# Kernel optimization log

Hardware: AMD Instinct MI355X
Metric: run time of the kernel (lower is better)

## Reference

```python
import jax, jax.numpy as jnp
import numpy as np

N_NODES = 100000
N_EDGES = 1600000
EMBED_DIM = 64


def setup_inputs() -> dict:
    key = jax.random.key(0)
    k1, k2, k3, k4 = jax.random.split(key, 4)
    ego_embeddings = jax.random.normal(k1, (N_NODES, EMBED_DIM), dtype=jnp.float32)
    adj_values = jax.random.uniform(k2, (N_EDGES,), dtype=jnp.float32)
    adj_rows = jax.random.randint(k3, (N_EDGES,), 0, N_NODES, dtype=jnp.int32)
    adj_cols = jax.random.randint(k4, (N_EDGES,), 0, N_NODES, dtype=jnp.int32)
    return {
        "ego_embeddings": ego_embeddings,
        "adj_values": adj_values,
        "adj_rows": adj_rows,
        "adj_cols": adj_cols,
    }


def reference(ego_embeddings, adj_values, adj_rows, adj_cols):
    # out[r, :] = sum_{e : rows[e]==r} values[e] * ego_embeddings[cols[e], :]
    # == tf.sparse.sparse_dense_matmul(adj, ego_embeddings)
    messages = adj_values[:, None] * ego_embeddings[adj_cols]  # [E, D]
    out = jax.ops.segment_sum(messages, adj_rows, num_segments=N_NODES)  # [N, D]
    return out
```

## Files before the change

### kernel.cpp

```cpp
#include <hip/hip_runtime.h>

#define N_NODES 100000
#define N_EDGES 1600000
#define EMBED_DIM 64

#define RPB 256
#define NBKT ((N_NODES + RPB - 1) / RPB)
#define CAP 4608
#define TILE 4096
#define NTILE ((N_EDGES + TILE - 1) / TILE)
#define OVCAP 8192

#define BG_THREADS 1024
#define EPT ((CAP + BG_THREADS - 1) / BG_THREADS)

__global__ __launch_bounds__(512) void k_binA(const int* __restrict__ rows,
                                              const int* __restrict__ cols,
                                              const float* __restrict__ vals,
                                              int* __restrict__ gcur,
                                              int2* __restrict__ packed,
                                              int* __restrict__ ov_cnt,
                                              int4* __restrict__ ov) {
    __shared__ int hist[NBKT];
    __shared__ int off[NBKT];
    __shared__ int cur[NBKT];
    __shared__ int gbase[NBKT];
    __shared__ int wsum[8];
    __shared__ int stotal;
    __shared__ int2 stage[TILE];
    __shared__ int dg[TILE];
    const int tid = threadIdx.x;
    const int lane = tid & 63;
    const int wid = tid >> 6;
    const int e0 = blockIdx.x * TILE;

    for (int i = tid; i < NBKT; i += 512) hist[i] = 0;
    __syncthreads();

    for (int i = tid; i < TILE; i += 512) {
        int e = e0 + i;
        if (e < N_EDGES) atomicAdd(&hist[rows[e] >> 8], 1);
    }
    __syncthreads();

    int v = (tid < NBKT) ? hist[tid] : 0;
    int incl = v;
    for (int o = 1; o < 64; o <<= 1) {
        int t = __shfl_up(incl, o, 64);
        if (lane >= o) incl += t;
    }
    if (lane == 63) wsum[wid] = incl;
    __syncthreads();
    if (wid == 0 && lane < 8) {
        int s = wsum[lane];
        int si = s;
        for (int o = 1; o < 8; o <<= 1) {
            int t = __shfl_up(si, o, 64);
            if (lane >= o) si += t;
        }
        wsum[lane] = si - s;
        if (lane == 7) stotal = si;
    }
    __syncthreads();
    int excl = incl - v + wsum[wid];
    if (tid < NBKT) { off[tid] = excl; cur[tid] = excl; }

    for (int b = tid; b < NBKT; b += 512) {
        int c = hist[b];
        gbase[b] = c ? atomicAdd(&gcur[b], c) : 0;
    }
    __syncthreads();

    for (int i = tid; i < TILE; i += 512) {
        int e = e0 + i;
        if (e < N_EDGES) {
            int r = rows[e];
            int b = r >> 8;
            int p = atomicAdd(&cur[b], 1);
            stage[p] = make_int2(((r & (RPB - 1)) << 17) | cols[e],
                                 __float_as_int(vals[e]));
            int d = gbase[b] + (p - off[b]);
            dg[p] = (d < CAP) ? (b * CAP + d) : (0x40000000 | b);
        }
    }
    __syncthreads();

    int total = stotal;
    for (int j = tid; j < total; j += 512) {
        int d = dg[j];
        int2 ev = stage[j];
        if (d & 0x40000000) {
            int b = d & 0xFFFF;
            int ovi = atomicAdd(ov_cnt, 1);
            if (ovi < OVCAP) {
                int r = b * RPB + (((unsigned)ev.x) >> 17);
                ov[ovi] = make_int4(r, ev.x & 0x1FFFF, ev.y, 0);
            }
        } else {
            packed[d] = ev;
        }
    }
}

__global__ __launch_bounds__(BG_THREADS) void k_bg(const float* __restrict__ x,
                                                   const int* __restrict__ gcur,
                                                   const int2* __restrict__ packed,
                                                   float* __restrict__ out) {
    __shared__ int2 stage[CAP];
    __shared__ int h[RPB];
    __shared__ int ofs[RPB];
    __shared__ int cur[RPB];
    __shared__ int wsum[4];
    const int b = blockIdx.x;
    const int tid = threadIdx.x;
    const int lane = tid & 63;
    const int wid = tid >> 6;
    int n = gcur[b];
    if (n > CAP) n = CAP;
    const int base = b * CAP;

    if (tid < RPB) h[tid] = 0;
    __syncthreads();

    int2 ereg[EPT];
    int lr[EPT];
#pragma unroll
    for (int jj = 0; jj < EPT; ++jj) {
        int j = tid + jj * BG_THREADS;
        lr[jj] = -1;
        if (j < n) {
            int2 e = packed[base + j];
            ereg[jj] = e;
            int r = ((unsigned)e.x) >> 17;
            lr[jj] = r;
            atomicAdd(&h[r], 1);
        }
    }
    __syncthreads();

    int hv = (tid < RPB) ? h[tid] : 0;
    int incl = hv;
    for (int o = 1; o < 64; o <<= 1) {
        int t = __shfl_up(incl, o, 64);
        if (lane >= o) incl += t;
    }
    if (tid < RPB && lane == 63) wsum[wid] = incl;
    __syncthreads();
    if (wid == 0 && lane < 4) {
        int s = wsum[lane];
        int si = s;
        for (int o = 1; o < 4; o <<= 1) {
            int t = __shfl_up(si, o, 64);
            if (lane >= o) si += t;
        }
        wsum[lane] = si - s;
    }
    __syncthreads();
    if (tid < RPB) {
        int o2 = incl - hv + wsum[wid];
        ofs[tid] = o2;
        cur[tid] = o2;
    }
    __syncthreads();

#pragma unroll
    for (int jj = 0; jj < EPT; ++jj) {
        if (lr[jj] >= 0) {
            int p = atomicAdd(&cur[lr[jj]], 1);
            stage[p] = ereg[jj];
        }
    }
    __syncthreads();

    const int half = lane >> 5;
    const int hl = lane & 31;
    const float2* __restrict__ x2 = (const float2*)x;
    for (int i = 0; i < 16; ++i) {
        int r = wid * 16 + i;
        int grow = b * RPB + r;
        if (grow >= N_NODES) break;
        int deg = h[r];
        int beg = ofs[r];
        float ax = 0.f, ay = 0.f;
        for (int j0 = 0; j0 < deg; j0 += 16) {
            float vv[8];
            float2 xv[8];
#pragma unroll
            for (int k = 0; k < 8; ++k) {
                int j = j0 + 2 * k + half;
                int2 e = (j < deg) ? stage[beg + j] : make_int2(0, 0);
                vv[k] = __int_as_float(e.y);
                xv[k] = x2[(e.x & 0x1FFFF) * 32 + hl];
            }
#pragma unroll
            for (int k = 0; k < 8; ++k) {
                ax += vv[k] * xv[k].x;
                ay += vv[k] * xv[k].y;
            }
        }
        ax += __shfl_xor(ax, 32);
        ay += __shfl_xor(ay, 32);
        if (half == 0) {
            ((float2*)out)[(size_t)grow * 32 + hl] = make_float2(ax, ay);
        }
    }
}

__global__ __launch_bounds__(256) void k_overflow(const float* __restrict__ x,
                                                  const int* __restrict__ ov_cnt,
                                                  const int4* __restrict__ ov,
                                                  float* __restrict__ out) {
    int n = *ov_cnt;
    if (n > OVCAP) n = OVCAP;
    int lane = threadIdx.x & 63;
    int wglobal = (blockIdx.x * 256 + threadIdx.x) >> 6;
    for (int i = wglobal; i < n; i += 64 * 4) {
        int4 e = ov[i];
        atomicAdd(&out[e.x * EMBED_DIM + lane],
                  __int_as_float(e.z) * x[e.y * EMBED_DIM + lane]);
    }
}

__global__ __launch_bounds__(256) void spmm_scatter_kernel(
    const float* __restrict__ x, const float* __restrict__ vals,
    const int* __restrict__ rows, const int* __restrict__ cols,
    float* __restrict__ out) {
    const int wave_in_block = threadIdx.x >> 6;
    const int lane = threadIdx.x & 63;
    const int e = blockIdx.x * 4 + wave_in_block;
    if (e >= N_EDGES) return;
    const float m = vals[e] * x[cols[e] * EMBED_DIM + lane];
    atomicAdd(&out[rows[e] * EMBED_DIM + lane], m);
}

extern "C" void kernel_launch(void* const* d_in, const int* in_sizes, int n_in,
                              void* d_out, int out_size, void* d_ws, size_t ws_size,
                              hipStream_t stream) {
    const float* x    = (const float*)d_in[0];
    const float* vals = (const float*)d_in[1];
    const int*   rows = (const int*)d_in[2];
    const int*   cols = (const int*)d_in[3];
    float* out = (float*)d_out;

    const size_t packed_b = (size_t)NBKT * CAP * 8;
    const size_t ov_b     = (size_t)OVCAP * 16;
    const size_t need = packed_b + ov_b + ((size_t)NBKT + 1) * 4;
    if (ws_size < need) {
        hipMemsetAsync(out, 0, (size_t)out_size * sizeof(float), stream);
        spmm_scatter_kernel<<<(N_EDGES + 3) / 4, 256, 0, stream>>>(x, vals, rows, cols, out);
        return;
    }

    int2* packed  = (int2*)d_ws;
    int4* ov      = (int4*)((char*)d_ws + packed_b);
    int*  gcur    = (int*)((char*)d_ws + packed_b + ov_b);
    int*  ov_cnt  = gcur + NBKT;

    hipMemsetAsync(gcur, 0, ((size_t)NBKT + 1) * sizeof(int), stream);

    k_binA<<<NTILE, 512, 0, stream>>>(rows, cols, vals, gcur, packed, ov_cnt, ov);
    k_bg<<<NBKT, BG_THREADS, 0, stream>>>(x, gcur, (const int2*)packed, out);
    k_overflow<<<64, 256, 0, stream>>>(x, ov_cnt, ov, out);
}
```

Before: 170.5 us.

## Fuse binning, bucket gather and overflow passes into one cooperative kernel

Replaces the memset plus three separate kernel launches with one cooperative kernel. It zeroes the counters, bins edges into row buckets and then runs the per-bucket gather, using grid-wide syncs between the phases. Each block now handles overflow edges for its own bucket, and the binning loads of rows, cols and vals are vectorized as int4/float4. This removes launch gaps and separate kernel boundaries. In exchange, all 391 blocks of 1024 threads must be co-resident, grid.sync has its own cost, and every block scans the whole overflow list. The old multi-kernel path is kept as a fallback if the cooperative launch fails.

```diff
diff --git a/kernel.cpp b/kernel.cpp
--- a/kernel.cpp
+++ b/kernel.cpp
@@ -1,4 +1,7 @@
 #include <hip/hip_runtime.h>
+#include <hip/hip_cooperative_groups.h>
+
+namespace cg = cooperative_groups;
 
 #define N_NODES 100000
 #define N_EDGES 1600000
@@ -10,9 +13,249 @@
 #define TILE 4096
 #define NTILE ((N_EDGES + TILE - 1) / TILE)
 #define OVCAP 8192
-
-#define BG_THREADS 1024
-#define EPT ((CAP + BG_THREADS - 1) / BG_THREADS)
+#define EPT 5
+
+#define SM_A_STAGE 6336
+#define SM_A_DG    (SM_A_STAGE + TILE * 8)
+#define SM_BYTES   (SM_A_DG + TILE * 4)
+#define SM_B_STAGE 3200
+
+__global__ __launch_bounds__(1024, 8) void k_fused(const int* __restrict__ rows,
+                                                   const int* __restrict__ cols,
+                                                   const float* __restrict__ vals,
+                                                   int* __restrict__ gcur,
+                                                   int2* __restrict__ packed,
+                                                   int* __restrict__ ov_cnt,
+                                                   int4* __restrict__ ov,
+                                                   const float* __restrict__ x,
+                                                   float* __restrict__ out) {
+    __shared__ __align__(16) char smem[SM_BYTES];
+    cg::grid_group grid = cg::this_grid();
+    const int tid = threadIdx.x;
+    const int lane = tid & 63;
+    const int wid = tid >> 6;
+    const int blk = blockIdx.x;
+
+    {
+        int gtid = blk * 1024 + tid;
+        if (gtid < NBKT + 1) gcur[gtid] = 0;
+    }
+    grid.sync();
+
+    {
+        int* hist  = (int*)smem;
+        int* off   = hist + NBKT;
+        int* cur   = off + NBKT;
+        int* gbase = cur + NBKT;
+        int* wsum  = gbase + NBKT;
+        int* stot  = wsum + 16;
+        int2* stage = (int2*)(smem + SM_A_STAGE);
+        int*  dg    = (int*)(smem + SM_A_DG);
+
+        for (int i = tid; i < NBKT; i += 1024) hist[i] = 0;
+        __syncthreads();
+
+        const int e0 = blk * TILE;
+        const int eb = e0 + 4 * tid;
+        int rr0 = -1, rr1 = -1, rr2 = -1, rr3 = -1;
+        if (eb + 3 < N_EDGES) {
+            int4 r4 = *(const int4*)(rows + eb);
+            rr0 = r4.x; rr1 = r4.y; rr2 = r4.z; rr3 = r4.w;
+        } else {
+            if (eb + 0 < N_EDGES) rr0 = rows[eb + 0];
+            if (eb + 1 < N_EDGES) rr1 = rows[eb + 1];
+            if (eb + 2 < N_EDGES) rr2 = rows[eb + 2];
+            if (eb + 3 < N_EDGES) rr3 = rows[eb + 3];
+        }
+        if (rr0 >= 0) atomicAdd(&hist[rr0 >> 8], 1);
+        if (rr1 >= 0) atomicAdd(&hist[rr1 >> 8], 1);
+        if (rr2 >= 0) atomicAdd(&hist[rr2 >> 8], 1);
+        if (rr3 >= 0) atomicAdd(&hist[rr3 >> 8], 1);
+        __syncthreads();
+
+        int v = (tid < NBKT) ? hist[tid] : 0;
+        int incl = v;
+        for (int o = 1; o < 64; o <<= 1) {
+            int t = __shfl_up(incl, o, 64);
+            if (lane >= o) incl += t;
+        }
+        if (lane == 63) wsum[wid] = incl;
+        __syncthreads();
+        if (wid == 0 && lane < 16) {
+            int s = wsum[lane];
+            int si = s;
+            for (int o = 1; o < 16; o <<= 1) {
+                int t = __shfl_up(si, o, 64);
+                if (lane >= o) si += t;
+            }
+            wsum[lane] = si - s;
+            if (lane == 15) *stot = si;
+        }
+        __syncthreads();
+        int excl = incl - v + wsum[wid];
+        if (tid < NBKT) { off[tid] = excl; cur[tid] = excl; }
+
+        for (int b = tid; b < NBKT; b += 1024) {
+            int c = hist[b];
+            gbase[b] = c ? atomicAdd(&gcur[b], c) : 0;
+        }
+        __syncthreads();
+
+        int cc0 = 0, cc1 = 0, cc2 = 0, cc3 = 0;
+        float vv0 = 0.f, vv1 = 0.f, vv2 = 0.f, vv3 = 0.f;
+        if (eb + 3 < N_EDGES) {
+            int4 c4 = *(const int4*)(cols + eb);
+            float4 v4 = *(const float4*)(vals + eb);
+            cc0 = c4.x; cc1 = c4.y; cc2 = c4.z; cc3 = c4.w;
+            vv0 = v4.x; vv1 = v4.y; vv2 = v4.z; vv3 = v4.w;
+        } else {
+            if (eb + 0 < N_EDGES) { cc0 = cols[eb + 0]; vv0 = vals[eb + 0]; }
+            if (eb + 1 < N_EDGES) { cc1 = cols[eb + 1]; vv1 = vals[eb + 1]; }
+            if (eb + 2 < N_EDGES) { cc2 = cols[eb + 2]; vv2 = vals[eb + 2]; }
+            if (eb + 3 < N_EDGES) { cc3 = cols[eb + 3]; vv3 = vals[eb + 3]; }
+        }
+#define PLACE(RR, CC, VV)                                                     \
+        if (RR >= 0) {                                                        \
+            int b_ = RR >> 8;                                                 \
+            int p_ = atomicAdd(&cur[b_], 1);                                  \
+            stage[p_] = make_int2(((RR & (RPB - 1)) << 17) | CC,              \
+                                  __float_as_int(VV));                        \
+            int d_ = gbase[b_] + (p_ - off[b_]);                              \
+            dg[p_] = (d_ < CAP) ? (b_ * CAP + d_) : (0x40000000 | b_);        \
+        }
+        PLACE(rr0, cc0, vv0)
+        PLACE(rr1, cc1, vv1)
+        PLACE(rr2, cc2, vv2)
+        PLACE(rr3, cc3, vv3)
+#undef PLACE
+        __syncthreads();
+
+        int total = *stot;
+        for (int j = tid; j < total; j += 1024) {
+            int d = dg[j];
+            int2 ev = stage[j];
+            if (d & 0x40000000) {
+                int b_ = d & 0xFFFF;
+                int ovi = atomicAdd(ov_cnt, 1);
+                if (ovi < OVCAP) {
+                    int r = b_ * RPB + (((unsigned)ev.x) >> 17);
+                    ov[ovi] = make_int4(r, ev.x & 0x1FFFF, ev.y, 0);
+                }
+            } else {
+                packed[d] = ev;
+            }
+        }
+    }
+    grid.sync();
+
+    {
+        int* h    = (int*)smem;
+        int* ofs  = h + RPB;
+        int* cur  = ofs + RPB;
+        int* wsum = cur + RPB;
+        int2* stage = (int2*)(smem + SM_B_STAGE);
+        const int b = blk;
+        int n = gcur[b];
+        if (n > CAP) n = CAP;
+        const int base = b * CAP;
+
+        if (tid < RPB) h[tid] = 0;
+        __syncthreads();
+
+        int2 ereg[EPT];
+        int lr[EPT];
+#pragma unroll
+        for (int jj = 0; jj < EPT; ++jj) {
+            int j = tid + jj * 1024;
+            lr[jj] = -1;
+            if (j < n) {
+                int2 e = packed[base + j];
+                ereg[jj] = e;
+                int r = ((unsigned)e.x) >> 17;
+                lr[jj] = r;
+                atomicAdd(&h[r], 1);
+            }
+        }
+        __syncthreads();
+
+        int hv = (tid < RPB) ? h[tid] : 0;
+        int incl = hv;
+        for (int o = 1; o < 64; o <<= 1) {
+            int t = __shfl_up(incl, o, 64);
+            if (lane >= o) incl += t;
+        }
+        if (tid < RPB && lane == 63) wsum[wid] = incl;
+        __syncthreads();
+        if (wid == 0 && lane < 4) {
+            int s = wsum[lane];
+            int si = s;
+            for (int o = 1; o < 4; o <<= 1) {
+                int t = __shfl_up(si, o, 64);
+                if (lane >= o) si += t;
+            }
+            wsum[lane] = si - s;
+        }
+        __syncthreads();
+        if (tid < RPB) {
+            int o2 = incl - hv + wsum[wid];
+            ofs[tid] = o2;
+            cur[tid] = o2;
+        }
+        __syncthreads();
+
+#pragma unroll
+        for (int jj = 0; jj < EPT; ++jj) {
+            if (lr[jj] >= 0) {
+                int p = atomicAdd(&cur[lr[jj]], 1);
+                stage[p] = ereg[jj];
+            }
+        }
+        __syncthreads();
+
+        const int half = lane >> 5;
+        const int hl = lane & 31;
+        const float2* __restrict__ x2 = (const float2*)x;
+        for (int i = 0; i < 16; ++i) {
+            int r = wid * 16 + i;
+            int grow = b * RPB + r;
+            if (grow >= N_NODES) break;
+            int deg = h[r];
+            int beg = ofs[r];
+            float ax = 0.f, ay = 0.f;
+            for (int j0 = 0; j0 < deg; j0 += 16) {
+                float pv[8];
+                float2 xv[8];
+#pragma unroll
+                for (int k = 0; k < 8; ++k) {
+                    int j = j0 + 2 * k + half;
+                    int2 e = (j < deg) ? stage[beg + j] : make_int2(0, 0);
+                    pv[k] = __int_as_float(e.y);
+                    xv[k] = x2[(e.x & 0x1FFFF) * 32 + hl];
+                }
+#pragma unroll
+                for (int k = 0; k < 8; ++k) {
+                    ax += pv[k] * xv[k].x;
+                    ay += pv[k] * xv[k].y;
+                }
+            }
+            ax += __shfl_xor(ax, 32);
+            ay += __shfl_xor(ay, 32);
+            if (half == 0) {
+                ((float2*)out)[(size_t)grow * 32 + hl] = make_float2(ax, ay);
+            }
+        }
+
+        int nov = *ov_cnt;
+        if (nov > OVCAP) nov = OVCAP;
+        for (int i = wid; i < nov; i += 16) {
+            int4 e = ov[i];
+            if ((e.x >> 8) == b) {
+                atomicAdd(&out[(size_t)e.x * EMBED_DIM + lane],
+                          __int_as_float(e.z) * x[(size_t)e.y * EMBED_DIM + lane]);
+            }
+        }
+    }
+}
 
 __global__ __launch_bounds__(512) void k_binA(const int* __restrict__ rows,
                                               const int* __restrict__ cols,
@@ -36,13 +279,11 @@
 
     for (int i = tid; i < NBKT; i += 512) hist[i] = 0;
     __syncthreads();
-
     for (int i = tid; i < TILE; i += 512) {
         int e = e0 + i;
         if (e < N_EDGES) atomicAdd(&hist[rows[e] >> 8], 1);
     }
     __syncthreads();
-
     int v = (tid < NBKT) ? hist[tid] : 0;
     int incl = v;
     for (int o = 1; o < 64; o <<= 1) {
@@ -64,13 +305,11 @@
     __syncthreads();
     int excl = incl - v + wsum[wid];
     if (tid < NBKT) { off[tid] = excl; cur[tid] = excl; }
-
     for (int b = tid; b < NBKT; b += 512) {
         int c = hist[b];
         gbase[b] = c ? atomicAdd(&gcur[b], c) : 0;
     }
     __syncthreads();
-
     for (int i = tid; i < TILE; i += 512) {
         int e = e0 + i;
         if (e < N_EDGES) {
@@ -84,7 +323,6 @@
         }
     }
     __syncthreads();
-
     int total = stotal;
     for (int j = tid; j < total; j += 512) {
         int d = dg[j];
@@ -102,10 +340,10 @@
     }
 }
 
-__global__ __launch_bounds__(BG_THREADS) void k_bg(const float* __restrict__ x,
-                                                   const int* __restrict__ gcur,
-                                                   const int2* __restrict__ packed,
-                                                   float* __restrict__ out) {
+__global__ __launch_bounds__(1024) void k_bg(const float* __restrict__ x,
+                                             const int* __restrict__ gcur,
+                                             const int2* __restrict__ packed,
+                                             float* __restrict__ out) {
     __shared__ int2 stage[CAP];
     __shared__ int h[RPB];
     __shared__ int ofs[RPB];
@@ -121,12 +359,11 @@
 
     if (tid < RPB) h[tid] = 0;
     __syncthreads();
-
     int2 ereg[EPT];
     int lr[EPT];
 #pragma unroll
     for (int jj = 0; jj < EPT; ++jj) {
-        int j = tid + jj * BG_THREADS;
+        int j = tid + jj * 1024;
         lr[jj] = -1;
         if (j < n) {
             int2 e = packed[base + j];
@@ -137,7 +374,6 @@
         }
     }
     __syncthreads();
-
     int hv = (tid < RPB) ? h[tid] : 0;
     int incl = hv;
     for (int o = 1; o < 64; o <<= 1) {
@@ -162,7 +398,6 @@
         cur[tid] = o2;
     }
     __syncthreads();
-
 #pragma unroll
     for (int jj = 0; jj < EPT; ++jj) {
         if (lr[jj] >= 0) {
@@ -171,7 +406,6 @@
         }
     }
     __syncthreads();
-
     const int half = lane >> 5;
     const int hl = lane & 31;
     const float2* __restrict__ x2 = (const float2*)x;
@@ -183,19 +417,19 @@
         int beg = ofs[r];
         float ax = 0.f, ay = 0.f;
         for (int j0 = 0; j0 < deg; j0 += 16) {
-            float vv[8];
+            float pv[8];
             float2 xv[8];
 #pragma unroll
             for (int k = 0; k < 8; ++k) {
                 int j = j0 + 2 * k + half;
                 int2 e = (j < deg) ? stage[beg + j] : make_int2(0, 0);
-                vv[k] = __int_as_float(e.y);
+                pv[k] = __int_as_float(e.y);
                 xv[k] = x2[(e.x & 0x1FFFF) * 32 + hl];
             }
 #pragma unroll
             for (int k = 0; k < 8; ++k) {
-                ax += vv[k] * xv[k].x;
-                ay += vv[k] * xv[k].y;
+                ax += pv[k] * xv[k].x;
+                ay += pv[k] * xv[k].y;
             }
         }
         ax += __shfl_xor(ax, 32);
@@ -236,10 +470,10 @@
 extern "C" void kernel_launch(void* const* d_in, const int* in_sizes, int n_in,
                               void* d_out, int out_size, void* d_ws, size_t ws_size,
                               hipStream_t stream) {
-    const float* x    = (const float*)d_in[0];
-    const float* vals = (const float*)d_in[1];
     const int*   rows = (const int*)d_in[2];
     const int*   cols = (const int*)d_in[3];
+    const float* vals = (const float*)d_in[1];
+    const float* x    = (const float*)d_in[0];
     float* out = (float*)d_out;
 
     const size_t packed_b = (size_t)NBKT * CAP * 8;
@@ -256,9 +490,16 @@
     int*  gcur    = (int*)((char*)d_ws + packed_b + ov_b);
     int*  ov_cnt  = gcur + NBKT;
 
+    void* args[] = { (void*)&rows, (void*)&cols, (void*)&vals, (void*)&gcur,
+                     (void*)&packed, (void*)&ov_cnt, (void*)&ov, (void*)&x,
+                     (void*)&out };
+    hipError_t err = hipLaunchCooperativeKernel((const void*)k_fused,
+                                                dim3(NBKT), dim3(1024),
+                                                args, 0, stream);
+    if (err == hipSuccess) return;
+
     hipMemsetAsync(gcur, 0, ((size_t)NBKT + 1) * sizeof(int), stream);
-
     k_binA<<<NTILE, 512, 0, stream>>>(rows, cols, vals, gcur, packed, ov_cnt, ov);
-    k_bg<<<NBKT, BG_THREADS, 0, stream>>>(x, gcur, (const int2*)packed, out);
+    k_bg<<<NBKT, 1024, 0, stream>>>(x, gcur, (const int2*)packed, out);
     k_overflow<<<64, 256, 0, stream>>>(x, ov_cnt, ov, out);
 }
```

Result: slower. 258.5 us (+51.6%).

## Widen binning blocks with vectorized edge loads and fold overflow into gather kernel

Applied to the files above, without the earlier changes.

The binning kernel now runs 1024 threads per tile. Each thread loads four consecutive rows, cols and vals with int4/float4 loads instead of strided scalar loads, and the scan widens to 16 waves. The separate overflow kernel is removed. Each gather block now scans the whole overflow list after its main pass and applies only the entries that belong to its bucket, which saves a launch. The cost is that every block reads the overflow list, which is costly if overflow is large. Binning also has more atomic contention per block.

```diff
diff --git a/kernel.cpp b/kernel.cpp
--- a/kernel.cpp
+++ b/kernel.cpp
@@ -10,22 +10,20 @@
 #define TILE 4096
 #define NTILE ((N_EDGES + TILE - 1) / TILE)
 #define OVCAP 8192
-
-#define BG_THREADS 1024
-#define EPT ((CAP + BG_THREADS - 1) / BG_THREADS)
-
-__global__ __launch_bounds__(512) void k_binA(const int* __restrict__ rows,
-                                              const int* __restrict__ cols,
-                                              const float* __restrict__ vals,
-                                              int* __restrict__ gcur,
-                                              int2* __restrict__ packed,
-                                              int* __restrict__ ov_cnt,
-                                              int4* __restrict__ ov) {
+#define EPT 5
+
+__global__ __launch_bounds__(1024) void k_binA(const int* __restrict__ rows,
+                                               const int* __restrict__ cols,
+                                               const float* __restrict__ vals,
+                                               int* __restrict__ gcur,
+                                               int2* __restrict__ packed,
+                                               int* __restrict__ ov_cnt,
+                                               int4* __restrict__ ov) {
     __shared__ int hist[NBKT];
     __shared__ int off[NBKT];
     __shared__ int cur[NBKT];
     __shared__ int gbase[NBKT];
-    __shared__ int wsum[8];
+    __shared__ int wsum[16];
     __shared__ int stotal;
     __shared__ int2 stage[TILE];
     __shared__ int dg[TILE];
@@ -34,13 +32,24 @@
     const int wid = tid >> 6;
     const int e0 = blockIdx.x * TILE;
 
-    for (int i = tid; i < NBKT; i += 512) hist[i] = 0;
-    __syncthreads();
-
-    for (int i = tid; i < TILE; i += 512) {
-        int e = e0 + i;
-        if (e < N_EDGES) atomicAdd(&hist[rows[e] >> 8], 1);
-    }
+    for (int i = tid; i < NBKT; i += 1024) hist[i] = 0;
+    __syncthreads();
+
+    const int eb = e0 + 4 * tid;
+    int rr0 = -1, rr1 = -1, rr2 = -1, rr3 = -1;
+    if (eb + 3 < N_EDGES) {
+        int4 r4 = *(const int4*)(rows + eb);
+        rr0 = r4.x; rr1 = r4.y; rr2 = r4.z; rr3 = r4.w;
+    } else {
+        if (eb + 0 < N_EDGES) rr0 = rows[eb + 0];
+        if (eb + 1 < N_EDGES) rr1 = rows[eb + 1];
+        if (eb + 2 < N_EDGES) rr2 = rows[eb + 2];
+        if (eb + 3 < N_EDGES) rr3 = rows[eb + 3];
+    }
+    if (rr0 >= 0) atomicAdd(&hist[rr0 >> 8], 1);
+    if (rr1 >= 0) atomicAdd(&hist[rr1 >> 8], 1);
+    if (rr2 >= 0) atomicAdd(&hist[rr2 >> 8], 1);
+    if (rr3 >= 0) atomicAdd(&hist[rr3 >> 8], 1);
     __syncthreads();
 
     int v = (tid < NBKT) ? hist[tid] : 0;
@@ -51,49 +60,64 @@
     }
     if (lane == 63) wsum[wid] = incl;
     __syncthreads();
-    if (wid == 0 && lane < 8) {
+    if (wid == 0 && lane < 16) {
         int s = wsum[lane];
         int si = s;
-        for (int o = 1; o < 8; o <<= 1) {
+        for (int o = 1; o < 16; o <<= 1) {
             int t = __shfl_up(si, o, 64);
             if (lane >= o) si += t;
         }
         wsum[lane] = si - s;
-        if (lane == 7) stotal = si;
+        if (lane == 15) stotal = si;
     }
     __syncthreads();
     int excl = incl - v + wsum[wid];
     if (tid < NBKT) { off[tid] = excl; cur[tid] = excl; }
 
-    for (int b = tid; b < NBKT; b += 512) {
+    for (int b = tid; b < NBKT; b += 1024) {
         int c = hist[b];
         gbase[b] = c ? atomicAdd(&gcur[b], c) : 0;
     }
     __syncthreads();
 
-    for (int i = tid; i < TILE; i += 512) {
-        int e = e0 + i;
-        if (e < N_EDGES) {
-            int r = rows[e];
-            int b = r >> 8;
-            int p = atomicAdd(&cur[b], 1);
-            stage[p] = make_int2(((r & (RPB - 1)) << 17) | cols[e],
-                                 __float_as_int(vals[e]));
-            int d = gbase[b] + (p - off[b]);
-            dg[p] = (d < CAP) ? (b * CAP + d) : (0x40000000 | b);
-        }
-    }
+    int cc0 = 0, cc1 = 0, cc2 = 0, cc3 = 0;
+    float vv0 = 0.f, vv1 = 0.f, vv2 = 0.f, vv3 = 0.f;
+    if (eb + 3 < N_EDGES) {
+        int4 c4 = *(const int4*)(cols + eb);
+        float4 v4 = *(const float4*)(vals + eb);
+        cc0 = c4.x; cc1 = c4.y; cc2 = c4.z; cc3 = c4.w;
+        vv0 = v4.x; vv1 = v4.y; vv2 = v4.z; vv3 = v4.w;
+    } else {
+        if (eb + 0 < N_EDGES) { cc0 = cols[eb + 0]; vv0 = vals[eb + 0]; }
+        if (eb + 1 < N_EDGES) { cc1 = cols[eb + 1]; vv1 = vals[eb + 1]; }
+        if (eb + 2 < N_EDGES) { cc2 = cols[eb + 2]; vv2 = vals[eb + 2]; }
+        if (eb + 3 < N_EDGES) { cc3 = cols[eb + 3]; vv3 = vals[eb + 3]; }
+    }
+#define PLACE(RR, CC, VV)                                                     \
+    if (RR >= 0) {                                                            \
+        int b_ = RR >> 8;                                                     \
+        int p_ = atomicAdd(&cur[b_], 1);                                      \
+        stage[p_] = make_int2(((RR & (RPB - 1)) << 17) | CC,                  \
+                              __float_as_int(VV));                            \
+        int d_ = gbase[b_] + (p_ - off[b_]);                                  \
+        dg[p_] = (d_ < CAP) ? (b_ * CAP + d_) : (0x40000000 | b_);            \
+    }
+    PLACE(rr0, cc0, vv0)
+    PLACE(rr1, cc1, vv1)
+    PLACE(rr2, cc2, vv2)
+    PLACE(rr3, cc3, vv3)
+#undef PLACE
     __syncthreads();
 
     int total = stotal;
-    for (int j = tid; j < total; j += 512) {
+    for (int j = tid; j < total; j += 1024) {
         int d = dg[j];
         int2 ev = stage[j];
         if (d & 0x40000000) {
-            int b = d & 0xFFFF;
+            int b_ = d & 0xFFFF;
             int ovi = atomicAdd(ov_cnt, 1);
             if (ovi < OVCAP) {
-                int r = b * RPB + (((unsigned)ev.x) >> 17);
+                int r = b_ * RPB + (((unsigned)ev.x) >> 17);
                 ov[ovi] = make_int4(r, ev.x & 0x1FFFF, ev.y, 0);
             }
         } else {
@@ -102,10 +126,12 @@
     }
 }
 
-__global__ __launch_bounds__(BG_THREADS) void k_bg(const float* __restrict__ x,
-                                                   const int* __restrict__ gcur,
-                                                   const int2* __restrict__ packed,
-                                                   float* __restrict__ out) {
+__global__ __launch_bounds__(1024) void k_bg(const float* __restrict__ x,
+                                             const int* __restrict__ gcur,
+                                             const int2* __restrict__ packed,
+                                             const int* __restrict__ ov_cnt,
+                                             const int4* __restrict__ ov,
+                                             float* __restrict__ out) {
     __shared__ int2 stage[CAP];
     __shared__ int h[RPB];
     __shared__ int ofs[RPB];
@@ -126,7 +152,7 @@
     int lr[EPT];
 #pragma unroll
     for (int jj = 0; jj < EPT; ++jj) {
-        int j = tid + jj * BG_THREADS;
+        int j = tid + jj * 1024;
         lr[jj] = -1;
         if (j < n) {
             int2 e = packed[base + j];
@@ -183,19 +209,19 @@
         int beg = ofs[r];
         float ax = 0.f, ay = 0.f;
         for (int j0 = 0; j0 < deg; j0 += 16) {
-            float vv[8];
+            float pv[8];
             float2 xv[8];
 #pragma unroll
             for (int k = 0; k < 8; ++k) {
                 int j = j0 + 2 * k + half;
                 int2 e = (j < deg) ? stage[beg + j] : make_int2(0, 0);
-                vv[k] = __int_as_float(e.y);
+                pv[k] = __int_as_float(e.y);
                 xv[k] = x2[(e.x & 0x1FFFF) * 32 + hl];
             }
 #pragma unroll
             for (int k = 0; k < 8; ++k) {
-                ax += vv[k] * xv[k].x;
-                ay += vv[k] * xv[k].y;
+                ax += pv[k] * xv[k].x;
+                ay += pv[k] * xv[k].y;
             }
         }
         ax += __shfl_xor(ax, 32);
@@ -204,20 +230,16 @@
             ((float2*)out)[(size_t)grow * 32 + hl] = make_float2(ax, ay);
         }
     }
-}
-
-__global__ __launch_bounds__(256) void k_overflow(const float* __restrict__ x,
-                                                  const int* __restrict__ ov_cnt,
-                                                  const int4* __restrict__ ov,
-                                                  float* __restrict__ out) {
-    int n = *ov_cnt;
-    if (n > OVCAP) n = OVCAP;
-    int lane = threadIdx.x & 63;
-    int wglobal = (blockIdx.x * 256 + threadIdx.x) >> 6;
-    for (int i = wglobal; i < n; i += 64 * 4) {
+
+    __syncthreads();
+    int nov = *ov_cnt;
+    if (nov > OVCAP) nov = OVCAP;
+    for (int i = wid; i < nov; i += 16) {
         int4 e = ov[i];
-        atomicAdd(&out[e.x * EMBED_DIM + lane],
-                  __int_as_float(e.z) * x[e.y * EMBED_DIM + lane]);
+        if ((e.x >> 8) == b) {
+            atomicAdd(&out[(size_t)e.x * EMBED_DIM + lane],
+                      __int_as_float(e.z) * x[(size_t)e.y * EMBED_DIM + lane]);
+        }
     }
 }
 
@@ -258,7 +280,6 @@
 
     hipMemsetAsync(gcur, 0, ((size_t)NBKT + 1) * sizeof(int), stream);
 
-    k_binA<<<NTILE, 512, 0, stream>>>(rows, cols, vals, gcur, packed, ov_cnt, ov);
-    k_bg<<<NBKT, BG_THREADS, 0, stream>>>(x, gcur, (const int2*)packed, out);
-    k_overflow<<<64, 256, 0, stream>>>(x, ov_cnt, ov, out);
-}
+    k_binA<<<NTILE, 1024, 0, stream>>>(rows, cols, vals, gcur, packed, ov_cnt, ov);
+    k_bg<<<NBKT, 1024, 0, stream>>>(x, gcur, (const int2*)packed, ov_cnt, ov, out);
+}
```

Result: faster. 167.0 us (-2.0%).
